# Kernel tuning notes

Hardware: AMD Instinct MI355X
Metric: run time of the kernel (lower is better)

## Reference

```python
import jax, jax.numpy as jnp
import numpy as np

N, E = 25000, 400000
D, H, L = 64, 4, 3
DH = D  # per-head out dim (concat=False averages heads)
NODE_IN, EDGE_IN = 16, 4


def setup_inputs() -> dict:
    key = jax.random.key(0)
    ks = jax.random.split(key, 24)
    s = 0.05
    inp = {
        "node_feat_in": jax.random.normal(ks[0], (N, NODE_IN), jnp.float32),
        "edge_index_in": jax.random.randint(ks[1], (2, E), 0, N, jnp.int32),
        "edge_attr_in": jax.random.normal(ks[2], (E, EDGE_IN), jnp.float32),
        # initial embeddings
        "W_node": jax.random.normal(ks[3], (NODE_IN, D), jnp.float32) * s,
        "b_node": jnp.zeros((D,), jnp.float32),
        "W_edge": jax.random.normal(ks[4], (EDGE_IN, D), jnp.float32) * s,
        "b_edge": jnp.zeros((D,), jnp.float32),
        # GATv2Conv params, stacked over layers
        "Wl": jax.random.normal(ks[5], (L, D, H * DH), jnp.float32) * s,
        "bl": jnp.zeros((L, H * DH), jnp.float32),
        "Wr": jax.random.normal(ks[6], (L, D, H * DH), jnp.float32) * s,
        "br": jnp.zeros((L, H * DH), jnp.float32),
        "We": jax.random.normal(ks[7], (L, D, H * DH), jnp.float32) * s,
        "att": jax.random.normal(ks[8], (L, H, DH), jnp.float32) * s,
        "conv_b": jnp.zeros((L, D), jnp.float32),
        # LayerNorm
        "ln_g": jnp.ones((L, D), jnp.float32),
        "ln_b": jnp.zeros((L, D), jnp.float32),
        # edge update MLP: Linear(3D->D), ReLU, Linear(D->D)
        "euW1": jax.random.normal(ks[9], (L, 3 * D, D), jnp.float32) * s,
        "eub1": jnp.zeros((L, D), jnp.float32),
        "euW2": jax.random.normal(ks[10], (L, D, D), jnp.float32) * s,
        "eub2": jnp.zeros((L, D), jnp.float32),
    }
    return inp


def _layernorm(x, g, b, eps=1e-5):
    mu = x.mean(-1, keepdims=True)
    var = ((x - mu) ** 2).mean(-1, keepdims=True)
    return (x - mu) * jax.lax.rsqrt(var + eps) * g + b


def _gatv2_conv(x, e, row, col, Wl, bl, Wr, br, We, att, cb):
    # PyG GATv2Conv(concat=False, edge_dim=D), eval mode (no dropout),
    # add_self_loops=True with fill_value='mean' on edge_attr.
    n = x.shape[0]
    xl = (x @ Wl + bl).reshape(n, H, DH)  # source transform
    xr = (x @ Wr + br).reshape(n, H, DH)  # target transform
    # self-loop edge attr = per-target mean of incoming edge attrs
    cnt = jax.ops.segment_sum(jnp.ones((e.shape[0],), x.dtype), col, num_segments=n)
    e_loop = jax.ops.segment_sum(e, col, num_segments=n) / jnp.maximum(cnt, 1.0)[:, None]
    ee = (jnp.concatenate([e, e_loop], 0) @ We).reshape(-1, H, DH)
    loop = jnp.arange(n, dtype=row.dtype)
    rowf = jnp.concatenate([row, loop])
    colf = jnp.concatenate([col, loop])
    msg = xl[rowf] + xr[colf] + ee                      # [E+N, H, DH]
    score = jnp.sum(jax.nn.leaky_relu(msg, 0.2) * att, -1)  # [E+N, H]
    # segment softmax over incoming edges of each target node
    m = jax.ops.segment_max(score, colf, num_segments=n)
    a = jnp.exp(score - m[colf])
    a = a / jax.ops.segment_sum(a, colf, num_segments=n)[colf]
    out = jax.ops.segment_sum(a[..., None] * xl[rowf], colf, num_segments=n)  # [N,H,DH]
    return out.mean(1) + cb  # concat=False -> head mean, plus bias


def reference(node_feat_in, edge_index_in, edge_attr_in, W_node, b_node, W_edge,
              b_edge, Wl, bl, Wr, br, We, att, conv_b, ln_g, ln_b, euW1, eub1,
              euW2, eub2):
    row, col = edge_index_in[0], edge_index_in[1]
    x = jax.nn.relu(node_feat_in @ W_node + b_node)
    e = jax.nn.relu(edge_attr_in @ W_edge + b_edge)
    for i in range(L):
        upd = _gatv2_conv(x, e, row, col, Wl[i], bl[i], Wr[i], br[i], We[i],
                          att[i], conv_b[i])
        x = jax.nn.relu(_layernorm(x + upd, ln_g[i], ln_b[i]))
        eu_in = jnp.concatenate([x[row], x[col], e], -1)  # [E, 3D]
        e_upd = jax.nn.relu(eu_in @ euW1[i] + eub1[i]) @ euW2[i] + eub2[i]
        e = jax.nn.relu(e + e_upd)
    return x, e
```

## Files before the change

kernel.cpp:

```cpp
#include <hip/hip_runtime.h>
#include <hip/hip_bf16.h>
#include <cstdint>
#include <cstddef>

constexpr int kN  = 25000;
constexpr int kE  = 400000;
constexpr int kEN = kE + kN;
constexpr int kD  = 64;
constexpr int kH  = 4;
constexpr int kHD = 256;

typedef __attribute__((ext_vector_type(8))) short short8;
typedef __attribute__((ext_vector_type(4))) float f32x4;

__device__ __forceinline__ float lrelu02(float x){ return x > 0.f ? x : 0.2f*x; }
__device__ __forceinline__ unsigned short f2bf(float f){
  __hip_bfloat16 h = __float2bfloat16(f);
  return *reinterpret_cast<unsigned short*>(&h);
}
__device__ __forceinline__ float bf2f(unsigned short u){
  return __uint_as_float(((unsigned)u) << 16);
}
__device__ __forceinline__ float bf_lo(unsigned u){ return __uint_as_float(u << 16); }
__device__ __forceinline__ float bf_hi(unsigned u){ return __uint_as_float(u & 0xffff0000u); }
__device__ __forceinline__ unsigned pack_bf2(float a, float b){
  return ((unsigned)f2bf(a)) | (((unsigned)f2bf(b)) << 16);
}

__global__ void k_deg(const int* __restrict__ col, int* __restrict__ deg){
  int i = blockIdx.x*256 + threadIdx.x;
  if (i < kE) atomicAdd(&deg[col[i]], 1);
}

__global__ void k_scan(const int* __restrict__ deg, int* __restrict__ col_start){
  __shared__ int lds[1024];
  __shared__ int carry_s;
  int t = threadIdx.x;
  if (t == 0) carry_s = 0;
  __syncthreads();
  for (int base = 0; base < kN; base += 1024){
    int v = (base + t < kN) ? deg[base + t] : 0;
    lds[t] = v; __syncthreads();
    for (int off = 1; off < 1024; off <<= 1){
      int add = (t >= off) ? lds[t - off] : 0;
      __syncthreads();
      lds[t] += add;
      __syncthreads();
    }
    int incl = lds[t];
    int carry = carry_s;
    if (base + t < kN) col_start[base + t] = carry + incl - v;
    __syncthreads();
    if (t == 0) carry_s = carry + lds[1023];
    __syncthreads();
  }
  if (t == 0) col_start[kN] = carry_s;
}

__global__ void k_fill(const int* __restrict__ col, const int* __restrict__ col_start,
                       int* __restrict__ fill, int* __restrict__ edge_ids){
  int i = blockIdx.x*256 + threadIdx.x;
  if (i < kE){
    int c = col[i];
    int p = atomicAdd(&fill[c], 1);
    edge_ids[col_start[c] + p] = i;
  }
}

__global__ void k_permrc(const int* __restrict__ edge_ids, const int* __restrict__ row,
                         const int* __restrict__ col, int* __restrict__ rowp,
                         int2* __restrict__ rc2){
  int p = blockIdx.x*256 + threadIdx.x;
  if (p < kE){
    int eid = edge_ids[p];
    int r = row[eid], c = col[eid];
    rowp[p] = r;
    rc2[p] = make_int2(r, c);
  }
}

__global__ void k_prep(const float* __restrict__ We, unsigned short* __restrict__ WeT){
  int idx = blockIdx.x*256 + threadIdx.x;
  if (idx >= 3*256*64) return;
  int l = idx >> 14, j = (idx >> 6) & 255, k = idx & 63;
  WeT[idx] = f2bf(We[(size_t)l*16384 + k*256 + j]);
}

__global__ void k_prep2(const float* __restrict__ euW1, const float* __restrict__ euW2,
                        unsigned short* __restrict__ W1cT, unsigned short* __restrict__ W2T){
  int idx = blockIdx.x*256 + threadIdx.x;
  if (idx >= 3*64*64) return;
  int l = idx >> 12, rem = idx & 4095, d = rem >> 6, k = rem & 63;
  W1cT[idx] = f2bf(euW1[(size_t)l*192*64 + (size_t)(128+k)*64 + d]);
  W2T[idx]  = f2bf(euW2[(size_t)l*64*64  + (size_t)k*64 + d]);
}

__global__ void k_x0(const float* __restrict__ nf, const float* __restrict__ W,
                     const float* __restrict__ b, float* __restrict__ x){
  int i = blockIdx.x*256 + threadIdx.x;
  if (i >= kN*kD) return;
  int n = i >> 6, d = i & 63;
  float acc = b[d];
#pragma unroll
  for (int k = 0; k < 16; k++) acc += nf[n*16 + k] * W[k*64 + d];
  x[i] = fmaxf(acc, 0.f);
}

__global__ void k_e0p(const int* __restrict__ edge_ids,
                      const float* __restrict__ ea, const float* __restrict__ W,
                      const float* __restrict__ b,
                      unsigned short* __restrict__ ebf_perm){
  long long i = (long long)blockIdx.x*256 + threadIdx.x;
  if (i >= (long long)kE*kD) return;
  int p = (int)(i >> 6), d = (int)(i & 63);
  int eid = edge_ids[p];
  float acc = b[d];
#pragma unroll
  for (int k = 0; k < 4; k++) acc += ea[eid*4 + k] * W[k*64 + d];
  ebf_perm[i] = f2bf(fmaxf(acc, 0.f));
}

#define XLR_NPB 8
__global__ __launch_bounds__(256) void k_xlr(const float* __restrict__ x,
    const float* __restrict__ Wl, const float* __restrict__ bl,
    const float* __restrict__ Wr, const float* __restrict__ br,
    unsigned short* __restrict__ xl_bf, unsigned short* __restrict__ xr_bf){
  __shared__ float xs[XLR_NPB*64];
  int j = threadIdx.x;
  int n0 = blockIdx.x * XLR_NPB;
  for (int i = j; i < XLR_NPB*64; i += 256){
    int n = n0 + (i >> 6);
    xs[i] = (n < kN) ? x[(size_t)n*64 + (i & 63)] : 0.f;
  }
  __syncthreads();
  float accl[XLR_NPB], accr[XLR_NPB];
  float blv = bl[j], brv = br[j];
#pragma unroll
  for (int t = 0; t < XLR_NPB; t++){ accl[t] = blv; accr[t] = brv; }
  for (int k = 0; k < 64; k++){
    float wl = Wl[k*kHD + j], wr = Wr[k*kHD + j];
#pragma unroll
    for (int t = 0; t < XLR_NPB; t++){
      float xv = xs[t*64 + k];
      accl[t] += xv * wl; accr[t] += xv * wr;
    }
  }
#pragma unroll
  for (int t = 0; t < XLR_NPB; t++){
    int n = n0 + t;
    if (n < kN){
      xl_bf[(size_t)n*kHD + j] = f2bf(accl[t]);
      xr_bf[(size_t)n*kHD + j] = f2bf(accr[t]);
    }
  }
}

__global__ __launch_bounds__(256) void k_eloop(const unsigned short* __restrict__ ebf_perm,
    const int* __restrict__ col_start, unsigned short* __restrict__ eloop_bf){
  int wave = threadIdx.x >> 6, lane = threadIdx.x & 63;
  int n = blockIdx.x*4 + wave;
  if (n >= kN) return;
  int s0 = col_start[n], s1 = col_start[n+1];
  float acc = 0.f;
  for (int p = s0; p < s1; p++)
    acc += bf2f(ebf_perm[(size_t)p*64 + lane]);
  int dg = s1 - s0;
  eloop_bf[(size_t)n*64 + lane] = f2bf(acc / (float)(dg > 0 ? dg : 1));
}

struct STile {
  short8 b0, b1;
  uint2 xlu[4], xru[4];
};

__device__ __forceinline__ void s_load(int tile, STile& f, int e16, int kb, int h,
    const unsigned short* __restrict__ ebf_perm,
    const unsigned short* __restrict__ eloop_bf,
    const unsigned short* __restrict__ xl_bf,
    const unsigned short* __restrict__ xr_bf,
    const int2* __restrict__ rc2)
{
  int p = tile*16 + e16;
  int pc = (p < kEN) ? p : 0;
  bool isE = pc < kE;
  int2 rc;
  if (isE) rc = rc2[pc];
  else { rc.x = pc - kE; rc.y = pc - kE; }
  const unsigned short* erow = isE ? (ebf_perm + (size_t)pc*64)
                                   : (eloop_bf + (size_t)(pc - kE)*64);
  f.b0 = *(const short8*)(erow + kb*8);
  f.b1 = *(const short8*)(erow + 32 + kb*8);
  const unsigned short* xl_ = xl_bf + (size_t)rc.x*kHD + h*64;
  const unsigned short* xr_ = xr_bf + (size_t)rc.y*kHD + h*64;
#pragma unroll
  for (int mt = 0; mt < 4; mt++){
    f.xlu[mt] = *(const uint2*)(xl_ + mt*16 + kb*4);
    f.xru[mt] = *(const uint2*)(xr_ + mt*16 + kb*4);
  }
}

__device__ __forceinline__ void s_comp(int tile, const STile& f,
    const short8 A[4][2], const uint2 attp[4], int lane, int h,
    float* __restrict__ score)
{
  float sc = 0.f;
#pragma unroll
  for (int mt = 0; mt < 4; mt++){
    f32x4 acc = {0.f,0.f,0.f,0.f};
    acc = __builtin_amdgcn_mfma_f32_16x16x32_bf16(A[mt][0], f.b0, acc, 0, 0, 0);
    acc = __builtin_amdgcn_mfma_f32_16x16x32_bf16(A[mt][1], f.b1, acc, 0, 0, 0);
    sc += lrelu02(acc[0] + bf_lo(f.xlu[mt].x) + bf_lo(f.xru[mt].x)) * bf_lo(attp[mt].x);
    sc += lrelu02(acc[1] + bf_hi(f.xlu[mt].x) + bf_hi(f.xru[mt].x)) * bf_hi(attp[mt].x);
    sc += lrelu02(acc[2] + bf_lo(f.xlu[mt].y) + bf_lo(f.xru[mt].y)) * bf_lo(attp[mt].y);
    sc += lrelu02(acc[3] + bf_hi(f.xlu[mt].y) + bf_hi(f.xru[mt].y)) * bf_hi(attp[mt].y);
  }
  sc += __shfl_xor(sc, 16);
  sc += __shfl_xor(sc, 32);
  int wp = tile*16 + lane;
  if (lane < 16 && wp < kEN) score[(size_t)wp*kH + h] = sc;
}

__global__ __launch_bounds__(256, 4) void k_score_mfma(
    const unsigned short* __restrict__ ebf_perm,
    const unsigned short* __restrict__ eloop_bf,
    const unsigned short* __restrict__ xl_bf,
    const unsigned short* __restrict__ xr_bf,
    const int2* __restrict__ rc2,
    const unsigned short* __restrict__ WeT,
    const float* __restrict__ att,
    float* __restrict__ score)
{
  int lane = threadIdx.x & 63;
  int h    = threadIdx.x >> 6;
  int e16  = lane & 15;
  int kb   = lane >> 4;

  short8 A[4][2];
  uint2 attp[4];
#pragma unroll
  for (int mt = 0; mt < 4; mt++){
    const unsigned short* arow = WeT + (size_t)(h*64 + mt*16 + e16)*64 + kb*8;
    A[mt][0] = *(const short8*)(arow);
    A[mt][1] = *(const short8*)(arow + 32);
    f32x4 av = *(const f32x4*)(att + h*64 + mt*16 + kb*4);
    attp[mt].x = pack_bf2(av[0], av[1]);
    attp[mt].y = pack_bf2(av[2], av[3]);
  }

  constexpr int NT = (kEN + 15)/16;
  int nblk = gridDim.x;
  int vb = (blockIdx.x & 7)*(nblk >> 3) + (blockIdx.x >> 3);
  int cpb = (NT + nblk - 1)/nblk;
  int t0 = vb*cpb;
  int tend = min(t0 + cpb, NT);
  int t = t0;
  for (; t + 2 <= tend; t += 2){
    STile fA, fB;
    s_load(t,   fA, e16, kb, h, ebf_perm, eloop_bf, xl_bf, xr_bf, rc2);
    s_load(t+1, fB, e16, kb, h, ebf_perm, eloop_bf, xl_bf, xr_bf, rc2);
    s_comp(t,   fA, A, attp, lane, h, score);
    s_comp(t+1, fB, A, attp, lane, h, score);
  }
  if (t < tend){
    STile fA;
    s_load(t, fA, e16, kb, h, ebf_perm, eloop_bf, xl_bf, xr_bf, rc2);
    s_comp(t, fA, A, attp, lane, h, score);
  }
}

__global__ void k_segmax(const float* __restrict__ score,
    const int* __restrict__ col_start,
    float* __restrict__ aw, float* __restrict__ inv_s){
  int i = blockIdx.x*256 + threadIdx.x;
  if (i >= kN*kH) return;
  int n = i >> 2, h = i & 3;
  float selfsc = score[(size_t)(kE + n)*kH + h];
  float m = selfsc;
  int s0 = col_start[n], s1 = col_start[n+1];
  for (int p = s0; p < s1; p++)
    m = fmaxf(m, score[(size_t)p*kH + h]);
  float s = expf(selfsc - m);
  aw[(size_t)(kE + n)*kH + h] = s;
  for (int p = s0; p < s1; p++){
    float w = expf(score[(size_t)p*kH + h] - m);
    aw[(size_t)p*kH + h] = w;
    s += w;
  }
  inv_s[i] = 1.f / s;
}

__global__ __launch_bounds__(256) void k_agg_ln(
    const unsigned short* __restrict__ xl_bf, const float* __restrict__ aw,
    const float* __restrict__ inv_s,
    const int* __restrict__ rowp, const int* __restrict__ col_start,
    const float* __restrict__ conv_b, const float* __restrict__ ln_g,
    const float* __restrict__ ln_b, float* __restrict__ x){
  int n = blockIdx.x;
  int j = threadIdx.x, h = j >> 6, d = j & 63;
  float inv = inv_s[n*4 + h];
  float acc = aw[(size_t)(kE + n)*kH + h] * bf2f(xl_bf[(size_t)n*kHD + j]);
  int s0 = col_start[n], s1 = col_start[n+1];
  int p = s0;
  for (; p + 4 <= s1; p += 4){
    int r0 = rowp[p],   r1 = rowp[p+1], r2 = rowp[p+2], r3 = rowp[p+3];
    float a0 = aw[(size_t)p*kH + h],     a1 = aw[(size_t)(p+1)*kH + h];
    float a2 = aw[(size_t)(p+2)*kH + h], a3 = aw[(size_t)(p+3)*kH + h];
    float v0 = bf2f(xl_bf[(size_t)r0*kHD + j]);
    float v1 = bf2f(xl_bf[(size_t)r1*kHD + j]);
    float v2 = bf2f(xl_bf[(size_t)r2*kHD + j]);
    float v3 = bf2f(xl_bf[(size_t)r3*kHD + j]);
    acc += a0*v0; acc += a1*v1; acc += a2*v2; acc += a3*v3;
  }
  for (; p < s1; p++)
    acc += aw[(size_t)p*kH + h] * bf2f(xl_bf[(size_t)rowp[p]*kHD + j]);
  acc *= inv;

  __shared__ float lds[256];
  lds[j] = acc; __syncthreads();
  if (j < 64){
    float upd = (lds[d] + lds[64+d] + lds[128+d] + lds[192+d]) * 0.25f + conv_b[d];
    float y = x[(size_t)n*64 + d] + upd;
    float mu = y;
#pragma unroll
    for (int off = 32; off; off >>= 1) mu += __shfl_xor(mu, off);
    mu *= (1.f/64.f);
    float diff = y - mu;
    float var = diff * diff;
#pragma unroll
    for (int off = 32; off; off >>= 1) var += __shfl_xor(var, off);
    var *= (1.f/64.f);
    float out = diff * rsqrtf(var + 1e-5f) * ln_g[d] + ln_b[d];
    x[(size_t)n*64 + d] = fmaxf(out, 0.f);
  }
}

#define PQ_NPB 16
__global__ __launch_bounds__(256) void k_pq(const float* __restrict__ x,
    const float* __restrict__ W1, const float* __restrict__ b1,
    unsigned short* __restrict__ P_bf, unsigned short* __restrict__ Q_bf){
  __shared__ float xs[PQ_NPB*64];
  int tid = threadIdx.x;
  int j = tid & 63;
  int s = tid >> 6;
  int n0 = blockIdx.x * PQ_NPB;
  for (int i = tid; i < PQ_NPB*64; i += 256){
    int n = n0 + (i >> 6);
    xs[i] = (n < kN) ? x[(size_t)n*64 + (i & 63)] : 0.f;
  }
  __syncthreads();
  float accP[4], accQ[4];
  float b1v = b1[j];
#pragma unroll
  for (int t = 0; t < 4; t++){ accP[t] = b1v; accQ[t] = 0.f; }
  for (int k = 0; k < 64; k++){
    float wa = W1[k*64 + j];
    float wb = W1[(64 + k)*64 + j];
#pragma unroll
    for (int t = 0; t < 4; t++){
      float xv = xs[(s*4 + t)*64 + k];
      accP[t] += xv * wa; accQ[t] += xv * wb;
    }
  }
#pragma unroll
  for (int t = 0; t < 4; t++){
    int n = n0 + s*4 + t;
    if (n < kN){
      P_bf[(size_t)n*64 + j] = f2bf(accP[t]);
      Q_bf[(size_t)n*64 + j] = f2bf(accQ[t]);
    }
  }
}

__global__ __launch_bounds__(256) void k_mlp_mfma(
    unsigned short* __restrict__ ebf_perm,
    float* __restrict__ eout_scatter,
    const int* __restrict__ edge_ids,
    const unsigned short* __restrict__ P_bf, const unsigned short* __restrict__ Q_bf,
    const unsigned short* __restrict__ W1cT,
    const unsigned short* __restrict__ W2T,
    const float* __restrict__ b2,
    const int2* __restrict__ rc2)
{
  __shared__ unsigned short Hl[4][1024];
  int lane = threadIdx.x & 63, wv = threadIdx.x >> 6;
  int e16 = lane & 15, g = lane >> 4;
  int swz = (e16 & 7) << 4;
  char* Hw = (char*)Hl[wv];
  bool last = (eout_scatter != nullptr);

  short8 a1[4][2], a2[4][2];
#pragma unroll
  for (int mt = 0; mt < 4; mt++){
#pragma unroll
    for (int c = 0; c < 2; c++){
      a1[mt][c] = *(const short8*)(W1cT + (size_t)(mt*16 + e16)*64 + c*32 + g*8);
      a2[mt][c] = *(const short8*)(W2T  + (size_t)(mt*16 + e16)*64 + c*32 + g*8);
    }
  }
  f32x4 b2v[4];
#pragma unroll
  for (int mt = 0; mt < 4; mt++) b2v[mt] = *(const f32x4*)(b2 + mt*16 + g*4);

  constexpr int NT = kE/16;
  int nblk = gridDim.x;
  int vb = (blockIdx.x & 7)*(nblk >> 3) + (blockIdx.x >> 3);
  int cpb = (NT + nblk - 1)/nblk;
  int t0 = vb*cpb;
  int tend = min(t0 + cpb, NT);
  for (int tile = t0 + wv; tile < tend; tile += 4){
    int p = tile*16 + e16;
    int2 rc = rc2[p];
    const unsigned short* erow = ebf_perm + (size_t)p*64;
    short8 eb0 = *(const short8*)(erow + g*8);
    short8 eb1 = *(const short8*)(erow + 32 + g*8);
    const unsigned short* Pr = P_bf + (size_t)rc.x*64;
    const unsigned short* Qc = Q_bf + (size_t)rc.y*64;

#pragma unroll
    for (int mt = 0; mt < 4; mt++){
      f32x4 acc = {0.f,0.f,0.f,0.f};
      acc = __builtin_amdgcn_mfma_f32_16x16x32_bf16(a1[mt][0], eb0, acc, 0, 0, 0);
      acc = __builtin_amdgcn_mfma_f32_16x16x32_bf16(a1[mt][1], eb1, acc, 0, 0, 0);
      uint2 pu = *(const uint2*)(Pr + mt*16 + g*4);
      uint2 qu = *(const uint2*)(Qc + mt*16 + g*4);
      float h0 = fmaxf(acc[0] + bf_lo(pu.x) + bf_lo(qu.x), 0.f);
      float h1 = fmaxf(acc[1] + bf_hi(pu.x) + bf_hi(qu.x), 0.f);
      float h2 = fmaxf(acc[2] + bf_lo(pu.y) + bf_lo(qu.y), 0.f);
      float h3 = fmaxf(acc[3] + bf_hi(pu.y) + bf_hi(qu.y), 0.f);
      uint2 pk; pk.x = pack_bf2(h0, h1); pk.y = pack_bf2(h2, h3);
      *(uint2*)(Hw + (((e16 << 7) + (mt << 5) + (g << 3)) ^ swz)) = pk;
    }
    short8 hb0 = *(const short8*)(Hw + (((e16 << 7)      + (g << 4)) ^ swz));
    short8 hb1 = *(const short8*)(Hw + (((e16 << 7) + 64 + (g << 4)) ^ swz));

    int oe = last ? edge_ids[p] : 0;
#pragma unroll
    for (int mt = 0; mt < 4; mt++){
      f32x4 o = {0.f,0.f,0.f,0.f};
      o = __builtin_amdgcn_mfma_f32_16x16x32_bf16(a2[mt][0], hb0, o, 0, 0, 0);
      o = __builtin_amdgcn_mfma_f32_16x16x32_bf16(a2[mt][1], hb1, o, 0, 0, 0);
      size_t off = (size_t)p*64 + mt*16 + g*4;
      uint2 u = *(const uint2*)(ebf_perm + off);
      f32x4 eo;
      eo[0] = bf_lo(u.x); eo[1] = bf_hi(u.x); eo[2] = bf_lo(u.y); eo[3] = bf_hi(u.y);
      f32x4 ne;
      ne[0] = fmaxf(eo[0] + o[0] + b2v[mt][0], 0.f);
      ne[1] = fmaxf(eo[1] + o[1] + b2v[mt][1], 0.f);
      ne[2] = fmaxf(eo[2] + o[2] + b2v[mt][2], 0.f);
      ne[3] = fmaxf(eo[3] + o[3] + b2v[mt][3], 0.f);
      if (!last){
        uint2 po; po.x = pack_bf2(ne[0], ne[1]); po.y = pack_bf2(ne[2], ne[3]);
        *(uint2*)(ebf_perm + off) = po;
      } else {
        *(f32x4*)(eout_scatter + (size_t)oe*64 + mt*16 + g*4) = ne;
      }
    }
  }
}

extern "C" void kernel_launch(void* const* d_in, const int* in_sizes, int n_in,
                              void* d_out, int out_size, void* d_ws, size_t ws_size,
                              hipStream_t stream) {
  const float* node_feat = (const float*)d_in[0];
  const int*   edge_idx  = (const int*)d_in[1];
  const float* edge_attr = (const float*)d_in[2];
  const float* W_node = (const float*)d_in[3];
  const float* b_node = (const float*)d_in[4];
  const float* W_edge = (const float*)d_in[5];
  const float* b_edge = (const float*)d_in[6];
  const float* Wl   = (const float*)d_in[7];
  const float* bl   = (const float*)d_in[8];
  const float* Wr   = (const float*)d_in[9];
  const float* br   = (const float*)d_in[10];
  const float* We   = (const float*)d_in[11];
  const float* att  = (const float*)d_in[12];
  const float* cvb  = (const float*)d_in[13];
  const float* lng  = (const float*)d_in[14];
  const float* lnb  = (const float*)d_in[15];
  const float* euW1 = (const float*)d_in[16];
  const float* eub1 = (const float*)d_in[17];
  const float* euW2 = (const float*)d_in[18];
  const float* eub2 = (const float*)d_in[19];

  const int* row = edge_idx;
  const int* col = edge_idx + kE;

  float* x = (float*)d_out;
  float* e_out = (float*)d_out + (size_t)kN*kD;

  char* p = (char*)d_ws;
  auto carve = [&](size_t bytes)->void*{
    void* r = (void*)p;
    p += (bytes + 255) & ~(size_t)255;
    return r;
  };
  unsigned short* xl_bf    = (unsigned short*)carve((size_t)kN*kHD*2);
  unsigned short* xr_bf    = (unsigned short*)carve((size_t)kN*kHD*2);
  unsigned short* P_bf     = (unsigned short*)carve((size_t)kN*kD*2);
  unsigned short* Q_bf     = (unsigned short*)carve((size_t)kN*kD*2);
  unsigned short* ebf_perm = (unsigned short*)carve((size_t)kE*kD*2);
  unsigned short* eloop_bf = (unsigned short*)carve((size_t)kN*kD*2);
  unsigned short* WeT      = (unsigned short*)carve((size_t)3*kHD*kD*2);
  unsigned short* W1cT     = (unsigned short*)carve((size_t)3*kD*kD*2);
  unsigned short* W2T      = (unsigned short*)carve((size_t)3*kD*kD*2);
  float* score  = (float*)carve((size_t)kEN*kH*4);
  float* aw     = (float*)carve((size_t)kEN*kH*4);
  float* inv_s  = (float*)carve((size_t)kN*kH*4);
  int* deg      = (int*)carve((size_t)kN*4);
  int* col_start= (int*)carve((size_t)(kN+1)*4);
  int* fill     = (int*)carve((size_t)kN*4);
  int* edge_ids = (int*)carve((size_t)kE*4);
  int* rowp     = (int*)carve((size_t)kE*4);
  int2* rc2     = (int2*)carve((size_t)kE*8);

  hipMemsetAsync(deg, 0, (size_t)kN*4, stream);
  hipMemsetAsync(fill, 0, (size_t)kN*4, stream);
  k_deg<<<(kE+255)/256, 256, 0, stream>>>(col, deg);
  k_scan<<<1, 1024, 0, stream>>>(deg, col_start);
  k_fill<<<(kE+255)/256, 256, 0, stream>>>(col, col_start, fill, edge_ids);
  k_permrc<<<(kE+255)/256, 256, 0, stream>>>(edge_ids, row, col, rowp, rc2);

  k_prep<<<192, 256, 0, stream>>>(We, WeT);
  k_prep2<<<48, 256, 0, stream>>>(euW1, euW2, W1cT, W2T);
  k_x0<<<(kN*kD+255)/256, 256, 0, stream>>>(node_feat, W_node, b_node, x);
  k_e0p<<<(int)(((size_t)kE*kD+255)/256), 256, 0, stream>>>(edge_ids, edge_attr, W_edge,
                                                            b_edge, ebf_perm);

  for (int i = 0; i < 3; i++){
    const float* Wl_i  = Wl  + (size_t)i*kD*kHD;
    const float* bl_i  = bl  + (size_t)i*kHD;
    const float* Wr_i  = Wr  + (size_t)i*kD*kHD;
    const float* br_i  = br  + (size_t)i*kHD;
    const float* att_i = att + (size_t)i*kHD;
    const float* cvb_i = cvb + (size_t)i*kD;
    const float* lng_i = lng + (size_t)i*kD;
    const float* lnb_i = lnb + (size_t)i*kD;
    const float* W1_i  = euW1 + (size_t)i*192*64;
    const float* b1_i  = eub1 + (size_t)i*kD;
    const float* b2_i  = eub2 + (size_t)i*kD;
    const unsigned short* WeT_i  = WeT  + (size_t)i*kHD*kD;
    const unsigned short* W1cT_i = W1cT + (size_t)i*kD*kD;
    const unsigned short* W2T_i  = W2T  + (size_t)i*kD*kD;

    k_xlr<<<(kN + XLR_NPB - 1)/XLR_NPB, 256, 0, stream>>>(x, Wl_i, bl_i, Wr_i, br_i,
                                                          xl_bf, xr_bf);
    k_eloop<<<(kN + 3)/4, 256, 0, stream>>>(ebf_perm, col_start, eloop_bf);
    k_score_mfma<<<2048, 256, 0, stream>>>(ebf_perm, eloop_bf, xl_bf, xr_bf,
                                           rc2, WeT_i, att_i, score);
    k_segmax<<<(kN*kH + 255)/256, 256, 0, stream>>>(score, col_start, aw, inv_s);
    k_agg_ln<<<kN, 256, 0, stream>>>(xl_bf, aw, inv_s, rowp, col_start,
                                     cvb_i, lng_i, lnb_i, x);
    k_pq<<<(kN + PQ_NPB - 1)/PQ_NPB, 256, 0, stream>>>(x, W1_i, b1_i, P_bf, Q_bf);
    k_mlp_mfma<<<2048, 256, 0, stream>>>(ebf_perm, (i < 2) ? nullptr : e_out,
                                         edge_ids, P_bf, Q_bf, W1cT_i, W2T_i, b2_i,
                                         rc2);
  }
}
```

Measured before the change: 1.089 ms.

## Fuse GAT self-loop mean, scoring, online softmax, aggregation and LayerNorm per node

Replaces the per-layer sequence of eloop, edge-score MFMA, segment softmax and aggregate+LayerNorm kernels with a single persistent node-centric kernel. It processes each target node's incoming edges in 16-edge MFMA tiles, computes the self-loop mean edge attribute on the fly, and applies an online softmax while accumulating xl. This removes the score/aw/eloop intermediate buffers, their global round trips and three launches. The edge MLP kernel also switches to a simple grid-stride tile loop. In exchange, low-degree nodes leave MFMA tiles partly empty and each node carries block-wide syncs and shuffle reductions.

```diff
diff --git a/kernel.cpp b/kernel.cpp
--- a/kernel.cpp
+++ b/kernel.cpp
@@ -5,7 +5,6 @@
 
 constexpr int kN  = 25000;
 constexpr int kE  = 400000;
-constexpr int kEN = kE + kN;
 constexpr int kD  = 64;
 constexpr int kH  = 4;
 constexpr int kHD = 256;
@@ -155,80 +154,16 @@
   }
 }
 
-__global__ __launch_bounds__(256) void k_eloop(const unsigned short* __restrict__ ebf_perm,
-    const int* __restrict__ col_start, unsigned short* __restrict__ eloop_bf){
-  int wave = threadIdx.x >> 6, lane = threadIdx.x & 63;
-  int n = blockIdx.x*4 + wave;
-  if (n >= kN) return;
-  int s0 = col_start[n], s1 = col_start[n+1];
-  float acc = 0.f;
-  for (int p = s0; p < s1; p++)
-    acc += bf2f(ebf_perm[(size_t)p*64 + lane]);
-  int dg = s1 - s0;
-  eloop_bf[(size_t)n*64 + lane] = f2bf(acc / (float)(dg > 0 ? dg : 1));
-}
-
-struct STile {
-  short8 b0, b1;
-  uint2 xlu[4], xru[4];
-};
-
-__device__ __forceinline__ void s_load(int tile, STile& f, int e16, int kb, int h,
+__global__ __launch_bounds__(256) void k_gat_node(
     const unsigned short* __restrict__ ebf_perm,
-    const unsigned short* __restrict__ eloop_bf,
     const unsigned short* __restrict__ xl_bf,
     const unsigned short* __restrict__ xr_bf,
-    const int2* __restrict__ rc2)
-{
-  int p = tile*16 + e16;
-  int pc = (p < kEN) ? p : 0;
-  bool isE = pc < kE;
-  int2 rc;
-  if (isE) rc = rc2[pc];
-  else { rc.x = pc - kE; rc.y = pc - kE; }
-  const unsigned short* erow = isE ? (ebf_perm + (size_t)pc*64)
-                                   : (eloop_bf + (size_t)(pc - kE)*64);
-  f.b0 = *(const short8*)(erow + kb*8);
-  f.b1 = *(const short8*)(erow + 32 + kb*8);
-  const unsigned short* xl_ = xl_bf + (size_t)rc.x*kHD + h*64;
-  const unsigned short* xr_ = xr_bf + (size_t)rc.y*kHD + h*64;
-#pragma unroll
-  for (int mt = 0; mt < 4; mt++){
-    f.xlu[mt] = *(const uint2*)(xl_ + mt*16 + kb*4);
-    f.xru[mt] = *(const uint2*)(xr_ + mt*16 + kb*4);
-  }
-}
-
-__device__ __forceinline__ void s_comp(int tile, const STile& f,
-    const short8 A[4][2], const uint2 attp[4], int lane, int h,
-    float* __restrict__ score)
-{
-  float sc = 0.f;
-#pragma unroll
-  for (int mt = 0; mt < 4; mt++){
-    f32x4 acc = {0.f,0.f,0.f,0.f};
-    acc = __builtin_amdgcn_mfma_f32_16x16x32_bf16(A[mt][0], f.b0, acc, 0, 0, 0);
-    acc = __builtin_amdgcn_mfma_f32_16x16x32_bf16(A[mt][1], f.b1, acc, 0, 0, 0);
-    sc += lrelu02(acc[0] + bf_lo(f.xlu[mt].x) + bf_lo(f.xru[mt].x)) * bf_lo(attp[mt].x);
-    sc += lrelu02(acc[1] + bf_hi(f.xlu[mt].x) + bf_hi(f.xru[mt].x)) * bf_hi(attp[mt].x);
-    sc += lrelu02(acc[2] + bf_lo(f.xlu[mt].y) + bf_lo(f.xru[mt].y)) * bf_lo(attp[mt].y);
-    sc += lrelu02(acc[3] + bf_hi(f.xlu[mt].y) + bf_hi(f.xru[mt].y)) * bf_hi(attp[mt].y);
-  }
-  sc += __shfl_xor(sc, 16);
-  sc += __shfl_xor(sc, 32);
-  int wp = tile*16 + lane;
-  if (lane < 16 && wp < kEN) score[(size_t)wp*kH + h] = sc;
-}
-
-__global__ __launch_bounds__(256, 4) void k_score_mfma(
-    const unsigned short* __restrict__ ebf_perm,
-    const unsigned short* __restrict__ eloop_bf,
-    const unsigned short* __restrict__ xl_bf,
-    const unsigned short* __restrict__ xr_bf,
-    const int2* __restrict__ rc2,
+    const int* __restrict__ rowp,
+    const int* __restrict__ col_start,
     const unsigned short* __restrict__ WeT,
     const float* __restrict__ att,
-    float* __restrict__ score)
+    const float* __restrict__ conv_b, const float* __restrict__ ln_g,
+    const float* __restrict__ ln_b, float* __restrict__ x)
 {
   int lane = threadIdx.x & 63;
   int h    = threadIdx.x >> 6;
@@ -247,90 +182,178 @@
     attp[mt].y = pack_bf2(av[2], av[3]);
   }
 
-  constexpr int NT = (kEN + 15)/16;
-  int nblk = gridDim.x;
-  int vb = (blockIdx.x & 7)*(nblk >> 3) + (blockIdx.x >> 3);
-  int cpb = (NT + nblk - 1)/nblk;
-  int t0 = vb*cpb;
-  int tend = min(t0 + cpb, NT);
-  int t = t0;
-  for (; t + 2 <= tend; t += 2){
-    STile fA, fB;
-    s_load(t,   fA, e16, kb, h, ebf_perm, eloop_bf, xl_bf, xr_bf, rc2);
-    s_load(t+1, fB, e16, kb, h, ebf_perm, eloop_bf, xl_bf, xr_bf, rc2);
-    s_comp(t,   fA, A, attp, lane, h, score);
-    s_comp(t+1, fB, A, attp, lane, h, score);
-  }
-  if (t < tend){
-    STile fA;
-    s_load(t, fA, e16, kb, h, ebf_perm, eloop_bf, xl_bf, xr_bf, rc2);
-    s_comp(t, fA, A, attp, lane, h, score);
-  }
-}
-
-__global__ void k_segmax(const float* __restrict__ score,
-    const int* __restrict__ col_start,
-    float* __restrict__ aw, float* __restrict__ inv_s){
-  int i = blockIdx.x*256 + threadIdx.x;
-  if (i >= kN*kH) return;
-  int n = i >> 2, h = i & 3;
-  float selfsc = score[(size_t)(kE + n)*kH + h];
-  float m = selfsc;
-  int s0 = col_start[n], s1 = col_start[n+1];
-  for (int p = s0; p < s1; p++)
-    m = fmaxf(m, score[(size_t)p*kH + h]);
-  float s = expf(selfsc - m);
-  aw[(size_t)(kE + n)*kH + h] = s;
-  for (int p = s0; p < s1; p++){
-    float w = expf(score[(size_t)p*kH + h] - m);
-    aw[(size_t)p*kH + h] = w;
-    s += w;
-  }
-  inv_s[i] = 1.f / s;
-}
-
-__global__ __launch_bounds__(256) void k_agg_ln(
-    const unsigned short* __restrict__ xl_bf, const float* __restrict__ aw,
-    const float* __restrict__ inv_s,
-    const int* __restrict__ rowp, const int* __restrict__ col_start,
-    const float* __restrict__ conv_b, const float* __restrict__ ln_g,
-    const float* __restrict__ ln_b, float* __restrict__ x){
-  int n = blockIdx.x;
-  int j = threadIdx.x, h = j >> 6, d = j & 63;
-  float inv = inv_s[n*4 + h];
-  float acc = aw[(size_t)(kE + n)*kH + h] * bf2f(xl_bf[(size_t)n*kHD + j]);
-  int s0 = col_start[n], s1 = col_start[n+1];
-  int p = s0;
-  for (; p + 4 <= s1; p += 4){
-    int r0 = rowp[p],   r1 = rowp[p+1], r2 = rowp[p+2], r3 = rowp[p+3];
-    float a0 = aw[(size_t)p*kH + h],     a1 = aw[(size_t)(p+1)*kH + h];
-    float a2 = aw[(size_t)(p+2)*kH + h], a3 = aw[(size_t)(p+3)*kH + h];
-    float v0 = bf2f(xl_bf[(size_t)r0*kHD + j]);
-    float v1 = bf2f(xl_bf[(size_t)r1*kHD + j]);
-    float v2 = bf2f(xl_bf[(size_t)r2*kHD + j]);
-    float v3 = bf2f(xl_bf[(size_t)r3*kHD + j]);
-    acc += a0*v0; acc += a1*v1; acc += a2*v2; acc += a3*v3;
-  }
-  for (; p < s1; p++)
-    acc += aw[(size_t)p*kH + h] * bf2f(xl_bf[(size_t)rowp[p]*kHD + j]);
-  acc *= inv;
-
-  __shared__ float lds[256];
-  lds[j] = acc; __syncthreads();
-  if (j < 64){
-    float upd = (lds[d] + lds[64+d] + lds[128+d] + lds[192+d]) * 0.25f + conv_b[d];
-    float y = x[(size_t)n*64 + d] + upd;
-    float mu = y;
-#pragma unroll
-    for (int off = 32; off; off >>= 1) mu += __shfl_xor(mu, off);
-    mu *= (1.f/64.f);
-    float diff = y - mu;
-    float var = diff * diff;
-#pragma unroll
-    for (int off = 32; off; off >>= 1) var += __shfl_xor(var, off);
-    var *= (1.f/64.f);
-    float out = diff * rsqrtf(var + 1e-5f) * ln_g[d] + ln_b[d];
-    x[(size_t)n*64 + d] = fmaxf(out, 0.f);
+  __shared__ float hout[4][64];
+
+  for (int n = blockIdx.x; n < kN; n += gridDim.x){
+    int s0 = col_start[n], s1 = col_start[n+1];
+    int deg = s1 - s0;
+
+    float xr_f[16];
+    {
+      const unsigned short* xrp = xr_bf + (size_t)n*kHD + h*64;
+#pragma unroll
+      for (int mt = 0; mt < 4; mt++){
+        uint2 u = *(const uint2*)(xrp + mt*16 + kb*4);
+        xr_f[mt*4+0] = bf_lo(u.x); xr_f[mt*4+1] = bf_hi(u.x);
+        xr_f[mt*4+2] = bf_lo(u.y); xr_f[mt*4+3] = bf_hi(u.y);
+      }
+    }
+
+    float m = -3.0e38f, s_part = 0.f;
+    float acc[16], esum[16];
+#pragma unroll
+    for (int i = 0; i < 16; i++){ acc[i] = 0.f; esum[i] = 0.f; }
+
+    for (int p0 = s0; p0 < s1; p0 += 16){
+      int cnt = s1 - p0;
+      bool act = (e16 < cnt);
+      int p = p0 + (act ? e16 : 0);
+
+      short8 b0 = {0,0,0,0,0,0,0,0};
+      short8 b1 = {0,0,0,0,0,0,0,0};
+      int r = 0;
+      if (act){
+        const unsigned short* erow = ebf_perm + (size_t)p*64;
+        b0 = *(const short8*)(erow + kb*8);
+        b1 = *(const short8*)(erow + 32 + kb*8);
+        r = rowp[p];
+      }
+      const unsigned short* xlp = xl_bf + (size_t)r*kHD + h*64;
+      float xlf[16];
+#pragma unroll
+      for (int mt = 0; mt < 4; mt++){
+        uint2 u = *(const uint2*)(xlp + mt*16 + kb*4);
+        xlf[mt*4+0] = bf_lo(u.x); xlf[mt*4+1] = bf_hi(u.x);
+        xlf[mt*4+2] = bf_lo(u.y); xlf[mt*4+3] = bf_hi(u.y);
+      }
+#pragma unroll
+      for (int i = 0; i < 8; i++){
+        esum[i]   += bf2f((unsigned short)b0[i]);
+        esum[8+i] += bf2f((unsigned short)b1[i]);
+      }
+      float scp = 0.f;
+#pragma unroll
+      for (int mt = 0; mt < 4; mt++){
+        f32x4 c = {0.f,0.f,0.f,0.f};
+        c = __builtin_amdgcn_mfma_f32_16x16x32_bf16(A[mt][0], b0, c, 0, 0, 0);
+        c = __builtin_amdgcn_mfma_f32_16x16x32_bf16(A[mt][1], b1, c, 0, 0, 0);
+        scp += lrelu02(c[0] + xlf[mt*4+0] + xr_f[mt*4+0]) * bf_lo(attp[mt].x);
+        scp += lrelu02(c[1] + xlf[mt*4+1] + xr_f[mt*4+1]) * bf_hi(attp[mt].x);
+        scp += lrelu02(c[2] + xlf[mt*4+2] + xr_f[mt*4+2]) * bf_lo(attp[mt].y);
+        scp += lrelu02(c[3] + xlf[mt*4+3] + xr_f[mt*4+3]) * bf_hi(attp[mt].y);
+      }
+      scp += __shfl_xor(scp, 16);
+      scp += __shfl_xor(scp, 32);
+      float sc = act ? scp : -3.0e38f;
+      float tmax = sc;
+      tmax = fmaxf(tmax, __shfl_xor(tmax, 1));
+      tmax = fmaxf(tmax, __shfl_xor(tmax, 2));
+      tmax = fmaxf(tmax, __shfl_xor(tmax, 4));
+      tmax = fmaxf(tmax, __shfl_xor(tmax, 8));
+      if (tmax > m){
+        float scale = __expf(m - tmax);
+        s_part *= scale;
+#pragma unroll
+        for (int i = 0; i < 16; i++) acc[i] *= scale;
+        m = tmax;
+      }
+      float w = act ? __expf(sc - m) : 0.f;
+      s_part += w;
+#pragma unroll
+      for (int i = 0; i < 16; i++) acc[i] += w * xlf[i];
+    }
+
+#pragma unroll
+    for (int i = 0; i < 16; i++){
+      float v = esum[i];
+      v += __shfl_xor(v, 1); v += __shfl_xor(v, 2);
+      v += __shfl_xor(v, 4); v += __shfl_xor(v, 8);
+      esum[i] = v;
+    }
+    float invdeg = 1.f / (float)(deg > 0 ? deg : 1);
+    short8 mb0, mb1;
+#pragma unroll
+    for (int i = 0; i < 8; i++){
+      mb0[i] = (short)f2bf(esum[i]   * invdeg);
+      mb1[i] = (short)f2bf(esum[8+i] * invdeg);
+    }
+    float xlsf[16];
+    {
+      const unsigned short* xlsp = xl_bf + (size_t)n*kHD + h*64;
+#pragma unroll
+      for (int mt = 0; mt < 4; mt++){
+        uint2 u = *(const uint2*)(xlsp + mt*16 + kb*4);
+        xlsf[mt*4+0] = bf_lo(u.x); xlsf[mt*4+1] = bf_hi(u.x);
+        xlsf[mt*4+2] = bf_lo(u.y); xlsf[mt*4+3] = bf_hi(u.y);
+      }
+    }
+    {
+      float scp = 0.f;
+#pragma unroll
+      for (int mt = 0; mt < 4; mt++){
+        f32x4 c = {0.f,0.f,0.f,0.f};
+        c = __builtin_amdgcn_mfma_f32_16x16x32_bf16(A[mt][0], mb0, c, 0, 0, 0);
+        c = __builtin_amdgcn_mfma_f32_16x16x32_bf16(A[mt][1], mb1, c, 0, 0, 0);
+        scp += lrelu02(c[0] + xlsf[mt*4+0] + xr_f[mt*4+0]) * bf_lo(attp[mt].x);
+        scp += lrelu02(c[1] + xlsf[mt*4+1] + xr_f[mt*4+1]) * bf_hi(attp[mt].x);
+        scp += lrelu02(c[2] + xlsf[mt*4+2] + xr_f[mt*4+2]) * bf_lo(attp[mt].y);
+        scp += lrelu02(c[3] + xlsf[mt*4+3] + xr_f[mt*4+3]) * bf_hi(attp[mt].y);
+      }
+      scp += __shfl_xor(scp, 16);
+      scp += __shfl_xor(scp, 32);
+      float sc = scp;
+      if (sc > m){
+        float scale = __expf(m - sc);
+        s_part *= scale;
+#pragma unroll
+        for (int i = 0; i < 16; i++) acc[i] *= scale;
+        m = sc;
+      }
+      float w = __expf(sc - m);
+      if (e16 == 0){
+        s_part += w;
+#pragma unroll
+        for (int i = 0; i < 16; i++) acc[i] += w * xlsf[i];
+      }
+    }
+    float s = s_part;
+    s += __shfl_xor(s, 1); s += __shfl_xor(s, 2);
+    s += __shfl_xor(s, 4); s += __shfl_xor(s, 8);
+#pragma unroll
+    for (int i = 0; i < 16; i++){
+      float v = acc[i];
+      v += __shfl_xor(v, 1); v += __shfl_xor(v, 2);
+      v += __shfl_xor(v, 4); v += __shfl_xor(v, 8);
+      acc[i] = v;
+    }
+    float inv = 1.f / s;
+    if (e16 == 0){
+#pragma unroll
+      for (int mt = 0; mt < 4; mt++){
+        f32x4 o;
+        o[0] = acc[mt*4+0]*inv; o[1] = acc[mt*4+1]*inv;
+        o[2] = acc[mt*4+2]*inv; o[3] = acc[mt*4+3]*inv;
+        *(f32x4*)&hout[h][mt*16 + kb*4] = o;
+      }
+    }
+    __syncthreads();
+    if (threadIdx.x < 64){
+      int d = threadIdx.x;
+      float upd = (hout[0][d] + hout[1][d] + hout[2][d] + hout[3][d]) * 0.25f + conv_b[d];
+      float y = x[(size_t)n*64 + d] + upd;
+      float mu = y;
+#pragma unroll
+      for (int off = 32; off; off >>= 1) mu += __shfl_xor(mu, off);
+      mu *= (1.f/64.f);
+      float diff = y - mu;
+      float var = diff * diff;
+#pragma unroll
+      for (int off = 32; off; off >>= 1) var += __shfl_xor(var, off);
+      var *= (1.f/64.f);
+      float out = diff * rsqrtf(var + 1e-5f) * ln_g[d] + ln_b[d];
+      x[(size_t)n*64 + d] = fmaxf(out, 0.f);
+    }
+    __syncthreads();
   }
 }
 
@@ -401,13 +424,9 @@
 #pragma unroll
   for (int mt = 0; mt < 4; mt++) b2v[mt] = *(const f32x4*)(b2 + mt*16 + g*4);
 
-  constexpr int NT = kE/16;
-  int nblk = gridDim.x;
-  int vb = (blockIdx.x & 7)*(nblk >> 3) + (blockIdx.x >> 3);
-  int cpb = (NT + nblk - 1)/nblk;
-  int t0 = vb*cpb;
-  int tend = min(t0 + cpb, NT);
-  for (int tile = t0 + wv; tile < tend; tile += 4){
+  int wid = (blockIdx.x*256 + threadIdx.x) >> 6;
+  int nw  = (gridDim.x*256) >> 6;
+  for (int tile = wid; tile < kE/16; tile += nw){
     int p = tile*16 + e16;
     int2 rc = rc2[p];
     const unsigned short* erow = ebf_perm + (size_t)p*64;
@@ -499,13 +518,9 @@
   unsigned short* P_bf     = (unsigned short*)carve((size_t)kN*kD*2);
   unsigned short* Q_bf     = (unsigned short*)carve((size_t)kN*kD*2);
   unsigned short* ebf_perm = (unsigned short*)carve((size_t)kE*kD*2);
-  unsigned short* eloop_bf = (unsigned short*)carve((size_t)kN*kD*2);
   unsigned short* WeT      = (unsigned short*)carve((size_t)3*kHD*kD*2);
   unsigned short* W1cT     = (unsigned short*)carve((size_t)3*kD*kD*2);
   unsigned short* W2T      = (unsigned short*)carve((size_t)3*kD*kD*2);
-  float* score  = (float*)carve((size_t)kEN*kH*4);
-  float* aw     = (float*)carve((size_t)kEN*kH*4);
-  float* inv_s  = (float*)carve((size_t)kN*kH*4);
   int* deg      = (int*)carve((size_t)kN*4);
   int* col_start= (int*)carve((size_t)(kN+1)*4);
   int* fill     = (int*)carve((size_t)kN*4);
@@ -544,12 +559,8 @@
 
     k_xlr<<<(kN + XLR_NPB - 1)/XLR_NPB, 256, 0, stream>>>(x, Wl_i, bl_i, Wr_i, br_i,
                                                           xl_bf, xr_bf);
-    k_eloop<<<(kN + 3)/4, 256, 0, stream>>>(ebf_perm, col_start, eloop_bf);
-    k_score_mfma<<<2048, 256, 0, stream>>>(ebf_perm, eloop_bf, xl_bf, xr_bf,
-                                           rc2, WeT_i, att_i, score);
-    k_segmax<<<(kN*kH + 255)/256, 256, 0, stream>>>(score, col_start, aw, inv_s);
-    k_agg_ln<<<kN, 256, 0, stream>>>(xl_bf, aw, inv_s, rowp, col_start,
-                                     cvb_i, lng_i, lnb_i, x);
+    k_gat_node<<<2048, 256, 0, stream>>>(ebf_perm, xl_bf, xr_bf, rowp, col_start,
+                                         WeT_i, att_i, cvb_i, lng_i, lnb_i, x);
     k_pq<<<(kN + PQ_NPB - 1)/PQ_NPB, 256, 0, stream>>>(x, W1_i, b1_i, P_bf, Q_bf);
     k_mlp_mfma<<<2048, 256, 0, stream>>>(ebf_perm, (i < 2) ? nullptr : e_out,
                                          edge_ids, P_bf, Q_bf, W1cT_i, W2T_i, b2_i,
```

Measured after the change: 1.433 ms. 31.6% more time.

## Fuse segment softmax into aggregation+LayerNorm and switch to grid-stride tile schedules

Applied to the files above, without the earlier changes.

Removes the separate segmax kernel and the aw/inv_s buffers. The aggregation kernel now computes the per-node max, the exponentials and the normalisation inline, with one wavefront per node and vectorised uint2 loads of xl. This avoids writing and re-reading the attention weights each layer, at the cost of reading scores twice per node. The score and MLP kernels change from contiguous per-block chunks to grid-strided tiles, with software double-buffering in the score kernel, and the occupancy hint on the score kernel is dropped. The fused kernel also uses __expf instead of expf.

```diff
diff --git a/kernel.cpp b/kernel.cpp
--- a/kernel.cpp
+++ b/kernel.cpp
@@ -220,7 +220,7 @@
   if (lane < 16 && wp < kEN) score[(size_t)wp*kH + h] = sc;
 }
 
-__global__ __launch_bounds__(256, 4) void k_score_mfma(
+__global__ __launch_bounds__(256) void k_score_mfma(
     const unsigned short* __restrict__ ebf_perm,
     const unsigned short* __restrict__ eloop_bf,
     const unsigned short* __restrict__ xl_bf,
@@ -248,89 +248,102 @@
   }
 
   constexpr int NT = (kEN + 15)/16;
-  int nblk = gridDim.x;
-  int vb = (blockIdx.x & 7)*(nblk >> 3) + (blockIdx.x >> 3);
-  int cpb = (NT + nblk - 1)/nblk;
-  int t0 = vb*cpb;
-  int tend = min(t0 + cpb, NT);
-  int t = t0;
-  for (; t + 2 <= tend; t += 2){
-    STile fA, fB;
-    s_load(t,   fA, e16, kb, h, ebf_perm, eloop_bf, xl_bf, xr_bf, rc2);
-    s_load(t+1, fB, e16, kb, h, ebf_perm, eloop_bf, xl_bf, xr_bf, rc2);
-    s_comp(t,   fA, A, attp, lane, h, score);
-    s_comp(t+1, fB, A, attp, lane, h, score);
-  }
-  if (t < tend){
-    STile fA;
-    s_load(t, fA, e16, kb, h, ebf_perm, eloop_bf, xl_bf, xr_bf, rc2);
-    s_comp(t, fA, A, attp, lane, h, score);
-  }
-}
-
-__global__ void k_segmax(const float* __restrict__ score,
-    const int* __restrict__ col_start,
-    float* __restrict__ aw, float* __restrict__ inv_s){
-  int i = blockIdx.x*256 + threadIdx.x;
-  if (i >= kN*kH) return;
-  int n = i >> 2, h = i & 3;
-  float selfsc = score[(size_t)(kE + n)*kH + h];
-  float m = selfsc;
-  int s0 = col_start[n], s1 = col_start[n+1];
-  for (int p = s0; p < s1; p++)
-    m = fmaxf(m, score[(size_t)p*kH + h]);
-  float s = expf(selfsc - m);
-  aw[(size_t)(kE + n)*kH + h] = s;
-  for (int p = s0; p < s1; p++){
-    float w = expf(score[(size_t)p*kH + h] - m);
-    aw[(size_t)p*kH + h] = w;
-    s += w;
-  }
-  inv_s[i] = 1.f / s;
+  const int G = gridDim.x;
+  STile fA, fB;
+  int t0 = blockIdx.x;
+  if (t0 < NT) s_load(t0, fA, e16, kb, h, ebf_perm, eloop_bf, xl_bf, xr_bf, rc2);
+  for (int tile = t0; tile < NT; tile += 2*G){
+    int t1 = tile + G;
+    if (t1 < NT) s_load(t1, fB, e16, kb, h, ebf_perm, eloop_bf, xl_bf, xr_bf, rc2);
+    s_comp(tile, fA, A, attp, lane, h, score);
+    if (t1 < NT){
+      int t2 = tile + 2*G;
+      if (t2 < NT) s_load(t2, fA, e16, kb, h, ebf_perm, eloop_bf, xl_bf, xr_bf, rc2);
+      s_comp(t1, fB, A, attp, lane, h, score);
+    }
+  }
 }
 
 __global__ __launch_bounds__(256) void k_agg_ln(
-    const unsigned short* __restrict__ xl_bf, const float* __restrict__ aw,
-    const float* __restrict__ inv_s,
+    const unsigned short* __restrict__ xl_bf, const float* __restrict__ score,
     const int* __restrict__ rowp, const int* __restrict__ col_start,
     const float* __restrict__ conv_b, const float* __restrict__ ln_g,
     const float* __restrict__ ln_b, float* __restrict__ x){
-  int n = blockIdx.x;
-  int j = threadIdx.x, h = j >> 6, d = j & 63;
-  float inv = inv_s[n*4 + h];
-  float acc = aw[(size_t)(kE + n)*kH + h] * bf2f(xl_bf[(size_t)n*kHD + j]);
+  int wv = threadIdx.x >> 6, l = threadIdx.x & 63;
+  int n = blockIdx.x*4 + wv;
+  if (n >= kN) return;
+  int h = l >> 4;
   int s0 = col_start[n], s1 = col_start[n+1];
+
+  float sc_self = score[(size_t)(kE + n)*kH + h];
+  float m = sc_self;
+  for (int p = s0; p < s1; p++)
+    m = fmaxf(m, score[(size_t)p*kH + h]);
+
+  float w0 = __expf(sc_self - m);
+  float s = w0;
+  float a0, a1, a2, a3;
+  {
+    uint2 u = *(const uint2*)(xl_bf + (size_t)n*kHD + l*4);
+    a0 = w0*bf_lo(u.x); a1 = w0*bf_hi(u.x);
+    a2 = w0*bf_lo(u.y); a3 = w0*bf_hi(u.y);
+  }
   int p = s0;
   for (; p + 4 <= s1; p += 4){
-    int r0 = rowp[p],   r1 = rowp[p+1], r2 = rowp[p+2], r3 = rowp[p+3];
-    float a0 = aw[(size_t)p*kH + h],     a1 = aw[(size_t)(p+1)*kH + h];
-    float a2 = aw[(size_t)(p+2)*kH + h], a3 = aw[(size_t)(p+3)*kH + h];
-    float v0 = bf2f(xl_bf[(size_t)r0*kHD + j]);
-    float v1 = bf2f(xl_bf[(size_t)r1*kHD + j]);
-    float v2 = bf2f(xl_bf[(size_t)r2*kHD + j]);
-    float v3 = bf2f(xl_bf[(size_t)r3*kHD + j]);
-    acc += a0*v0; acc += a1*v1; acc += a2*v2; acc += a3*v3;
-  }
-  for (; p < s1; p++)
-    acc += aw[(size_t)p*kH + h] * bf2f(xl_bf[(size_t)rowp[p]*kHD + j]);
-  acc *= inv;
-
-  __shared__ float lds[256];
-  lds[j] = acc; __syncthreads();
-  if (j < 64){
-    float upd = (lds[d] + lds[64+d] + lds[128+d] + lds[192+d]) * 0.25f + conv_b[d];
-    float y = x[(size_t)n*64 + d] + upd;
-    float mu = y;
-#pragma unroll
-    for (int off = 32; off; off >>= 1) mu += __shfl_xor(mu, off);
-    mu *= (1.f/64.f);
-    float diff = y - mu;
-    float var = diff * diff;
-#pragma unroll
-    for (int off = 32; off; off >>= 1) var += __shfl_xor(var, off);
-    var *= (1.f/64.f);
-    float out = diff * rsqrtf(var + 1e-5f) * ln_g[d] + ln_b[d];
-    x[(size_t)n*64 + d] = fmaxf(out, 0.f);
+    float e0 = __expf(score[(size_t)(p+0)*kH + h] - m);
+    float e1 = __expf(score[(size_t)(p+1)*kH + h] - m);
+    float e2 = __expf(score[(size_t)(p+2)*kH + h] - m);
+    float e3 = __expf(score[(size_t)(p+3)*kH + h] - m);
+    int r0 = rowp[p], r1 = rowp[p+1], r2 = rowp[p+2], r3 = rowp[p+3];
+    uint2 u0 = *(const uint2*)(xl_bf + (size_t)r0*kHD + l*4);
+    uint2 u1 = *(const uint2*)(xl_bf + (size_t)r1*kHD + l*4);
+    uint2 u2 = *(const uint2*)(xl_bf + (size_t)r2*kHD + l*4);
+    uint2 u3 = *(const uint2*)(xl_bf + (size_t)r3*kHD + l*4);
+    s += e0 + e1 + e2 + e3;
+    a0 += e0*bf_lo(u0.x) + e1*bf_lo(u1.x) + e2*bf_lo(u2.x) + e3*bf_lo(u3.x);
+    a1 += e0*bf_hi(u0.x) + e1*bf_hi(u1.x) + e2*bf_hi(u2.x) + e3*bf_hi(u3.x);
+    a2 += e0*bf_lo(u0.y) + e1*bf_lo(u1.y) + e2*bf_lo(u2.y) + e3*bf_lo(u3.y);
+    a3 += e0*bf_hi(u0.y) + e1*bf_hi(u1.y) + e2*bf_hi(u2.y) + e3*bf_hi(u3.y);
+  }
+  for (; p < s1; p++){
+    float ew = __expf(score[(size_t)p*kH + h] - m);
+    int r = rowp[p];
+    uint2 u = *(const uint2*)(xl_bf + (size_t)r*kHD + l*4);
+    s += ew;
+    a0 += ew*bf_lo(u.x); a1 += ew*bf_hi(u.x);
+    a2 += ew*bf_lo(u.y); a3 += ew*bf_hi(u.y);
+  }
+  float inv = 1.f / s;
+  a0 *= inv; a1 *= inv; a2 *= inv; a3 *= inv;
+  a0 += __shfl_xor(a0, 16); a0 += __shfl_xor(a0, 32);
+  a1 += __shfl_xor(a1, 16); a1 += __shfl_xor(a1, 32);
+  a2 += __shfl_xor(a2, 16); a2 += __shfl_xor(a2, 32);
+  a3 += __shfl_xor(a3, 16); a3 += __shfl_xor(a3, 32);
+  int d0 = (l & 15)*4;
+  f32x4 cb = *(const f32x4*)(conv_b + d0);
+  f32x4 xv = *(const f32x4*)(x + (size_t)n*64 + d0);
+  float y0 = xv[0] + a0*0.25f + cb[0];
+  float y1 = xv[1] + a1*0.25f + cb[1];
+  float y2 = xv[2] + a2*0.25f + cb[2];
+  float y3 = xv[3] + a3*0.25f + cb[3];
+  float part = y0 + y1 + y2 + y3;
+  part += __shfl_xor(part, 1); part += __shfl_xor(part, 2);
+  part += __shfl_xor(part, 4); part += __shfl_xor(part, 8);
+  float mu = part * (1.f/64.f);
+  float f0 = y0 - mu, f1 = y1 - mu, f2 = y2 - mu, f3 = y3 - mu;
+  float vp = f0*f0 + f1*f1 + f2*f2 + f3*f3;
+  vp += __shfl_xor(vp, 1); vp += __shfl_xor(vp, 2);
+  vp += __shfl_xor(vp, 4); vp += __shfl_xor(vp, 8);
+  float rstd = rsqrtf(vp * (1.f/64.f) + 1e-5f);
+  f32x4 gv = *(const f32x4*)(ln_g + d0);
+  f32x4 bv = *(const f32x4*)(ln_b + d0);
+  if (l < 16){
+    f32x4 o;
+    o[0] = fmaxf(f0*rstd*gv[0] + bv[0], 0.f);
+    o[1] = fmaxf(f1*rstd*gv[1] + bv[1], 0.f);
+    o[2] = fmaxf(f2*rstd*gv[2] + bv[2], 0.f);
+    o[3] = fmaxf(f3*rstd*gv[3] + bv[3], 0.f);
+    *(f32x4*)(x + (size_t)n*64 + d0) = o;
   }
 }
 
@@ -401,13 +414,9 @@
 #pragma unroll
   for (int mt = 0; mt < 4; mt++) b2v[mt] = *(const f32x4*)(b2 + mt*16 + g*4);
 
-  constexpr int NT = kE/16;
-  int nblk = gridDim.x;
-  int vb = (blockIdx.x & 7)*(nblk >> 3) + (blockIdx.x >> 3);
-  int cpb = (NT + nblk - 1)/nblk;
-  int t0 = vb*cpb;
-  int tend = min(t0 + cpb, NT);
-  for (int tile = t0 + wv; tile < tend; tile += 4){
+  int wid = (blockIdx.x*256 + threadIdx.x) >> 6;
+  int nw  = (gridDim.x*256) >> 6;
+  for (int tile = wid; tile < kE/16; tile += nw){
     int p = tile*16 + e16;
     int2 rc = rc2[p];
     const unsigned short* erow = ebf_perm + (size_t)p*64;
@@ -504,8 +513,6 @@
   unsigned short* W1cT     = (unsigned short*)carve((size_t)3*kD*kD*2);
   unsigned short* W2T      = (unsigned short*)carve((size_t)3*kD*kD*2);
   float* score  = (float*)carve((size_t)kEN*kH*4);
-  float* aw     = (float*)carve((size_t)kEN*kH*4);
-  float* inv_s  = (float*)carve((size_t)kN*kH*4);
   int* deg      = (int*)carve((size_t)kN*4);
   int* col_start= (int*)carve((size_t)(kN+1)*4);
   int* fill     = (int*)carve((size_t)kN*4);
@@ -547,9 +554,8 @@
     k_eloop<<<(kN + 3)/4, 256, 0, stream>>>(ebf_perm, col_start, eloop_bf);
     k_score_mfma<<<2048, 256, 0, stream>>>(ebf_perm, eloop_bf, xl_bf, xr_bf,
                                            rc2, WeT_i, att_i, score);
-    k_segmax<<<(kN*kH + 255)/256, 256, 0, stream>>>(score, col_start, aw, inv_s);
-    k_agg_ln<<<kN, 256, 0, stream>>>(xl_bf, aw, inv_s, rowp, col_start,
-                                     cvb_i, lng_i, lnb_i, x);
+    k_agg_ln<<<(kN + 3)/4, 256, 0, stream>>>(xl_bf, score, rowp, col_start,
+                                             cvb_i, lng_i, lnb_i, x);
     k_pq<<<(kN + PQ_NPB - 1)/PQ_NPB, 256, 0, stream>>>(x, W1_i, b1_i, P_bf, Q_bf);
     k_mlp_mfma<<<2048, 256, 0, stream>>>(ebf_perm, (i < 2) ? nullptr : e_out,
                                          edge_ids, P_bf, Q_bf, W1cT_i, W2T_i, b2_i,
```

Result: faster. 986.1 us (-9.5%).
